# Performance work log

Hardware: AMD Instinct MI355X
Metric: run time of the kernel (lower is better)

The kernel has to match this reference:

```python
import jax, jax.numpy as jnp
import numpy as np

NEG_INF = -1e9
LRELU_SLOPE = 0.2  # torch GAT default leaky_relu negative slope


def setup_inputs() -> dict:
    key = jax.random.key(0)
    k1, k2, k3, k4, k5 = jax.random.split(key, 5)
    N, F_IN, H, DH = 4096, 1433, 8, 8  # n_nodes, in_features, n_heads, per-head dim (n_hidden=64)
    vert = jax.random.normal(k1, (N, F_IN), dtype=jnp.float32)
    edge = jax.random.randint(k2, (N, N), 0, 2, dtype=jnp.int32)  # dense adjacency mask
    W = jax.random.normal(k3, (F_IN, H * DH), dtype=jnp.float32) * 0.05
    a_l = jax.random.normal(k4, (H, DH), dtype=jnp.float32) * 0.05
    a_r = jax.random.normal(k5, (H, DH), dtype=jnp.float32) * 0.05
    return {"vert": vert, "edge": edge, "W": W, "a_l": a_l, "a_r": a_r}


def reference(vert, edge, W, a_l, a_r):
    # GAT-style edge-affinity layer (is_concat=True) + ELU; dropout is identity (eval mode).
    N = vert.shape[0]
    H, DH = a_l.shape
    g = (vert @ W).reshape(N, H, DH)                      # [N,H,Dh] projected node features
    sl = jnp.einsum('nhd,hd->nh', g, a_l)                 # source-node attention term
    sr = jnp.einsum('nhd,hd->nh', g, a_r)                 # target-node attention term
    e = sl[:, None, :] + sr[None, :, :]                   # [N,N,H]: attn([g_i || g_j])
    e = jnp.where(e >= 0, e, LRELU_SLOPE * e)             # leaky_relu
    mask = (edge != 0)[:, :, None]                        # [N,N,1]
    e = jnp.where(mask, e, NEG_INF)                       # mask non-edges
    a = jax.nn.softmax(e, axis=1)                         # normalize over neighbors j
    out = jnp.einsum('ijh,jhd->ihd', a, g).reshape(N, H * DH)  # aggregate + concat heads
    return jax.nn.elu(out)
```

## Files before the change

kernel.cpp:

```cpp
#include <hip/hip_runtime.h>
#include <hip/hip_bf16.h>

#define NN 4096
#define FIN 1433
#define NH 8
#define DH 8
#define HD 64
#define KP 1472
#define LOG2E 1.44269504f

typedef unsigned int u32;
typedef unsigned long long u64;
typedef float v4f __attribute__((ext_vector_type(4)));
typedef short bf16x4 __attribute__((ext_vector_type(4)));
typedef short bf16x8 __attribute__((ext_vector_type(8)));

static __device__ __forceinline__ short f2bf(float f) {
    union { __hip_bfloat16 h; short s; } u; u.h = __float2bfloat16(f); return u.s;
}

__global__ __launch_bounds__(256) void k_wprep(const float* __restrict__ W,
                                               short* __restrict__ Wt) {
    __shared__ float Ts[64][65];
    const int c = blockIdx.x;
    const int u = threadIdx.x;
    const int n4 = (u & 15) * 4;
    const int kr = u >> 4;
#pragma unroll
    for (int q = 0; q < 4; ++q) {
        const int kl = kr + q * 16;
        const int kg = c * 64 + kl;
        v4f v = {0.f, 0.f, 0.f, 0.f};
        if (kg < FIN) v = *(const v4f*)&W[(size_t)kg * HD + n4];
        *(v4f*)&Ts[kl][n4] = v;
    }
    __syncthreads();
    const int n = u >> 2;
    const int koff = (u & 3) * 16;
    __align__(16) short tmp[16];
#pragma unroll
    for (int r = 0; r < 16; ++r) tmp[r] = f2bf(Ts[koff + r][n]);
    *(uint4*)&Wt[(size_t)n * KP + c * 64 + koff]     = *(uint4*)&tmp[0];
    *(uint4*)&Wt[(size_t)n * KP + c * 64 + koff + 8] = *(uint4*)&tmp[8];
}

__global__ __launch_bounds__(256, 4) void k_gemm(
    const float* __restrict__ vert, const short* __restrict__ Wt,
    const float* __restrict__ al, const float* __restrict__ ar,
    short* __restrict__ gT, float* __restrict__ sl, float* __restrict__ srT)
{
    __shared__ float cacc[4][16][64];

    const int t = threadIdx.x, lane = t & 63, w = t >> 6;
    const int ml = lane & 15, q = lane >> 4;
    const int i0 = blockIdx.x * 16;
    const float* vrow = vert + (size_t)(i0 + ml) * FIN;

    v4f acc[4];
#pragma unroll
    for (int g = 0; g < 4; ++g) acc[g] = (v4f){0.f, 0.f, 0.f, 0.f};

    for (int c = w; c < 45; c += 4) {
        const int k0 = c * 32 + q * 8;
        v4f a0, a1;
        if (k0 + 7 < FIN) {
            a0 = *(const v4f*)&vrow[k0];
            a1 = *(const v4f*)&vrow[k0 + 4];
        } else {
            float tmp[8];
#pragma unroll
            for (int e = 0; e < 8; ++e)
                tmp[e] = (k0 + e < FIN) ? vrow[k0 + e] : 0.f;
            a0 = (v4f){tmp[0], tmp[1], tmp[2], tmp[3]};
            a1 = (v4f){tmp[4], tmp[5], tmp[6], tmp[7]};
        }
        const bf16x8 af = {f2bf(a0.x), f2bf(a0.y), f2bf(a0.z), f2bf(a0.w),
                           f2bf(a1.x), f2bf(a1.y), f2bf(a1.z), f2bf(a1.w)};
#pragma unroll
        for (int g = 0; g < 4; ++g) {
            const bf16x8 bf = *(const bf16x8*)&Wt[(size_t)(g * 16 + ml) * KP + k0];
            acc[g] = __builtin_amdgcn_mfma_f32_16x16x32_bf16(af, bf, acc[g], 0, 0, 0);
        }
    }

#pragma unroll
    for (int g = 0; g < 4; ++g)
#pragma unroll
        for (int r = 0; r < 4; ++r)
            cacc[w][q * 4 + r][g * 16 + ml] = acc[g][r];
    __syncthreads();

    const int m = t >> 4, n4 = (t & 15) * 4;
    v4f s = (v4f){0.f, 0.f, 0.f, 0.f};
#pragma unroll
    for (int ww = 0; ww < 4; ++ww) s += *(const v4f*)&cacc[ww][m][n4];

#pragma unroll
    for (int e = 0; e < 4; ++e)
        gT[(size_t)(n4 + e) * NN + i0 + m] = f2bf(s[e]);

    float pl = s.x * al[n4] + s.y * al[n4 + 1] + s.z * al[n4 + 2] + s.w * al[n4 + 3];
    float pr = s.x * ar[n4] + s.y * ar[n4 + 1] + s.z * ar[n4 + 2] + s.w * ar[n4 + 3];
    pl += __shfl_xor(pl, 1, 64);
    pr += __shfl_xor(pr, 1, 64);
    if ((t & 1) == 0) {
        const int h = (t & 15) >> 1;
        sl[(i0 + m) * NH + h]  = pl * LOG2E;
        srT[h * NN + i0 + m]   = pr * LOG2E;
    }
}

__global__ __launch_bounds__(256, 4) void k_attn(
    const int* __restrict__ edge, const short* __restrict__ gT,
    const float* __restrict__ sl, const float* __restrict__ srT,
    float* __restrict__ numw, float* __restrict__ denw)
{
    __shared__ __align__(16) short Gt[2][33][136];
    __shared__ __align__(16) float srs[2][4][132];
    __shared__ u32 mrow[2][16][5];

    const int t = threadIdx.x;
    const int lane = t & 63, w = t >> 6;
    const int ml = lane & 15, quad = lane >> 4;
    const int i0 = blockIdx.x * 16;
    const int hg = blockIdx.y;
    const int js = blockIdx.z;
    const int jbase = js * 2048;
    const int h  = hg * 4 + w;

    const float sli = sl[(i0 + ml) * NH + h];

    const int r2 = t >> 4, seg = (t & 15) * 8;
    const int shl = t >> 5 >= 4 ? 0 : t >> 5;
    const int sj4 = (t & 31) * 4;
    const int half = lane >> 5 ? 1 : 0;

    if (t < 16) {
        const u32 ones2 = 0x3f803f80u;
        uint4 o4 = {ones2, ones2, ones2, ones2};
        *(uint4*)&Gt[0][32][t * 8] = o4;
        *(uint4*)&Gt[1][32][t * 8] = o4;
    }

    const short* gTh = gT + (hg * 32) * NN;
    const float* srh = srT + (hg * 4) * NN;

    uint4 pg0, pg1; v4f psr; int pe[8];
    {
        pg0 = *(const uint4*)&gTh[r2 * NN + jbase + seg];
        pg1 = *(const uint4*)&gTh[(r2 + 16) * NN + jbase + seg];
        if (t < 128) psr = *(const v4f*)&srh[shl * NN + jbase + sj4];
#pragma unroll
        for (int rr = 0; rr < 4; ++rr) {
            pe[rr * 2]     = edge[(i0 + w * 4 + rr) * NN + jbase + (lane & 63)];
            pe[rr * 2 + 1] = edge[(i0 + w * 4 + rr) * NN + jbase + 64 + (lane & 63)];
        }
    }
    *(uint4*)&Gt[0][r2][seg]      = pg0;
    *(uint4*)&Gt[0][r2 + 16][seg] = pg1;
    if (t < 128) *(v4f*)&srs[0][shl][sj4] = psr;
#pragma unroll
    for (int rr = 0; rr < 4; ++rr) {
        u64 b0 = __ballot(pe[rr * 2] != 0);
        u64 b1 = __ballot(pe[rr * 2 + 1] != 0);
        if (lane == 0)  { mrow[0][w * 4 + rr][0] = (u32)b0;         mrow[0][w * 4 + rr][2] = (u32)b1; }
        if (lane == 32) { mrow[0][w * 4 + rr][1] = (u32)(b0 >> 32); mrow[0][w * 4 + rr][3] = (u32)(b1 >> 32); }
    }
    __syncthreads();

    v4f acc = {0.f, 0.f, 0.f, 0.f};

    for (int c = 0; c < 16; ++c) {
        const int cb = c & 1, nb = cb ^ 1;
        const bool pf = (c + 1) < 16;
        if (pf) {
            const int j0 = jbase + (c + 1) * 128;
            pg0 = *(const uint4*)&gTh[r2 * NN + j0 + seg];
            pg1 = *(const uint4*)&gTh[(r2 + 16) * NN + j0 + seg];
            if (t < 128) psr = *(const v4f*)&srh[shl * NN + j0 + sj4];
#pragma unroll
            for (int rr = 0; rr < 4; ++rr) {
                pe[rr * 2]     = edge[(i0 + w * 4 + rr) * NN + j0 + (lane & 63)];
                pe[rr * 2 + 1] = edge[(i0 + w * 4 + rr) * NN + j0 + 64 + (lane & 63)];
            }
        }
        const int brow = (ml < 8) ? (w * 8 + ml) : 32;
#pragma unroll
        for (int s = 0; s < 4; ++s) {
            const v4f s0 = *(const v4f*)&srs[cb][w][s * 32 + quad * 8];
            const v4f s1 = *(const v4f*)&srs[cb][w][s * 32 + quad * 8 + 4];
            const u32 mw = mrow[cb][ml][s] >> (quad * 8);
            const bf16x8 bfrag = *(const bf16x8*)&Gt[cb][brow][s * 32 + quad * 8];

            float e0 = sli + s0.x, e1 = sli + s0.y, e2 = sli + s0.z, e3 = sli + s0.w;
            float e4 = sli + s1.x, e5 = sli + s1.y, e6 = sli + s1.z, e7 = sli + s1.w;
            float p[8];
            p[0] = exp2f((mw & 1u)   ? fmaxf(e0, 0.2f * e0) : -1e9f);
            p[1] = exp2f((mw & 2u)   ? fmaxf(e1, 0.2f * e1) : -1e9f);
            p[2] = exp2f((mw & 4u)   ? fmaxf(e2, 0.2f * e2) : -1e9f);
            p[3] = exp2f((mw & 8u)   ? fmaxf(e3, 0.2f * e3) : -1e9f);
            p[4] = exp2f((mw & 16u)  ? fmaxf(e4, 0.2f * e4) : -1e9f);
            p[5] = exp2f((mw & 32u)  ? fmaxf(e5, 0.2f * e5) : -1e9f);
            p[6] = exp2f((mw & 64u)  ? fmaxf(e6, 0.2f * e6) : -1e9f);
            p[7] = exp2f((mw & 128u) ? fmaxf(e7, 0.2f * e7) : -1e9f);
            u32 w01 = __builtin_amdgcn_perm(__float_as_uint(p[1]), __float_as_uint(p[0]), 0x07060302u);
            u32 w23 = __builtin_amdgcn_perm(__float_as_uint(p[3]), __float_as_uint(p[2]), 0x07060302u);
            u32 w45 = __builtin_amdgcn_perm(__float_as_uint(p[5]), __float_as_uint(p[4]), 0x07060302u);
            u32 w67 = __builtin_amdgcn_perm(__float_as_uint(p[7]), __float_as_uint(p[6]), 0x07060302u);
            uint4 au = {w01, w23, w45, w67};
            const bf16x8 afrag = *(const bf16x8*)&au;
            acc = __builtin_amdgcn_mfma_f32_16x16x32_bf16(afrag, bfrag, acc, 0, 0, 0);
        }
        if (pf) {
            *(uint4*)&Gt[nb][r2][seg]      = pg0;
            *(uint4*)&Gt[nb][r2 + 16][seg] = pg1;
            if (t < 128) *(v4f*)&srs[nb][shl][sj4] = psr;
#pragma unroll
            for (int rr = 0; rr < 4; ++rr) {
                u64 b0 = __ballot(pe[rr * 2] != 0);
                u64 b1 = __ballot(pe[rr * 2 + 1] != 0);
                if (lane == 0)  { mrow[nb][w * 4 + rr][0] = (u32)b0;         mrow[nb][w * 4 + rr][2] = (u32)b1; }
                if (lane == 32) { mrow[nb][w * 4 + rr][1] = (u32)(b0 >> 32); mrow[nb][w * 4 + rr][3] = (u32)(b1 >> 32); }
            }
        }
        __syncthreads();
    }

    float* nw = numw + (size_t)js * NN * HD;
    float* dw = denw + (size_t)js * NN * NH;
    const int iA = i0 + quad * 4;
#pragma unroll
    for (int r = 0; r < 4; ++r) {
        if (ml < 8)       nw[(iA + r) * HD + h * 8 + ml] = acc[r];
        else if (ml == 8) dw[(iA + r) * NH + h]          = acc[r];
    }
}

__global__ __launch_bounds__(256) void k_comb(
    const float* __restrict__ numw, const float* __restrict__ denw,
    float* __restrict__ out)
{
    const int gid = blockIdx.x * 256 + threadIdx.x;
    const int i = gid >> 6, h = (gid & 63) >> 3;
    const float num = numw[gid] + numw[NN * HD + gid];
    const float den = denw[i * NH + h] + denw[NN * NH + i * NH + h];
    float x = num / den;
    out[gid] = (x > 0.f) ? x : (__expf(x) - 1.f);
}

extern "C" void kernel_launch(void* const* d_in, const int* in_sizes, int n_in,
                              void* d_out, int out_size, void* d_ws, size_t ws_size,
                              hipStream_t stream) {
    const float* vert = (const float*)d_in[0];
    const int*   edge = (const int*)d_in[1];
    const float* W    = (const float*)d_in[2];
    const float* al   = (const float*)d_in[3];
    const float* ar   = (const float*)d_in[4];
    float* out = (float*)d_out;

    char* ws = (char*)d_ws;
    short* gT   = (short*)ws;
    float* sl   = (float*)(ws + 512 * 1024);
    float* srT  = (float*)(ws + 640 * 1024);
    short* Wt   = (short*)(ws + 768 * 1024);
    float* numw = (float*)(ws + 1024 * 1024);
    float* denw = (float*)(ws + 3 * 1024 * 1024);

    hipLaunchKernelGGL(k_wprep, dim3(23), dim3(256), 0, stream, W, Wt);
    hipLaunchKernelGGL(k_gemm, dim3(NN / 16), dim3(256), 0, stream,
                       vert, Wt, al, ar, gT, sl, srT);
    hipLaunchKernelGGL(k_attn, dim3(NN / 16, 2, 2), dim3(256), 0, stream,
                       edge, gT, sl, srT, numw, denw);
    hipLaunchKernelGGL(k_comb, dim3(NN * HD / 256), dim3(256), 0, stream,
                       numw, denw, out);
}
```

Measured before the change: 172.5 us.

## Factor exp of leaky-relu scores into per-node products and split j four ways

The attention kernel now uses exp2(max(x,0.2x)) = max(exp2(x), exp2(0.2x)) and the additivity of the score. The GEMM kernel precomputes per-node exponentials (A,C for sources, B,D for targets), so the inner loop does two multiplies and a max instead of adds, leaky-relu and an exp2 per element. The neighbor dimension is also split into 4 partitions instead of 2, which gives more blocks, and the combine kernel sums four partials. The trade-offs are an extra shared-memory array and more global loads of target factors. Without max-subtraction the products may overflow or underflow if scores are large, and the reduction now touches twice as many partials.

```diff
diff --git a/kernel.cpp b/kernel.cpp
--- a/kernel.cpp
+++ b/kernel.cpp
@@ -8,6 +8,7 @@
 #define HD 64
 #define KP 1472
 #define LOG2E 1.44269504f
+#define NJS 4
 
 typedef unsigned int u32;
 typedef unsigned long long u64;
@@ -47,7 +48,8 @@
 __global__ __launch_bounds__(256, 4) void k_gemm(
     const float* __restrict__ vert, const short* __restrict__ Wt,
     const float* __restrict__ al, const float* __restrict__ ar,
-    short* __restrict__ gT, float* __restrict__ sl, float* __restrict__ srT)
+    short* __restrict__ gT, float2* __restrict__ eAC,
+    float* __restrict__ eB, float* __restrict__ eD)
 {
     __shared__ float cacc[4][16][64];
 
@@ -105,18 +107,22 @@
     pr += __shfl_xor(pr, 1, 64);
     if ((t & 1) == 0) {
         const int h = (t & 15) >> 1;
-        sl[(i0 + m) * NH + h]  = pl * LOG2E;
-        srT[h * NN + i0 + m]   = pr * LOG2E;
+        const int node = i0 + m;
+        eAC[node * NH + h] = make_float2(exp2f(pl * LOG2E), exp2f(0.2f * pl * LOG2E));
+        eB[h * NN + node] = exp2f(pr * LOG2E);
+        eD[h * NN + node] = exp2f(0.2f * pr * LOG2E);
     }
 }
 
 __global__ __launch_bounds__(256, 4) void k_attn(
     const int* __restrict__ edge, const short* __restrict__ gT,
-    const float* __restrict__ sl, const float* __restrict__ srT,
+    const float2* __restrict__ eAC, const float* __restrict__ eB,
+    const float* __restrict__ eD,
     float* __restrict__ numw, float* __restrict__ denw)
 {
     __shared__ __align__(16) short Gt[2][33][136];
-    __shared__ __align__(16) float srs[2][4][132];
+    __shared__ __align__(16) float srB[2][4][132];
+    __shared__ __align__(16) float srD[2][4][132];
     __shared__ u32 mrow[2][16][5];
 
     const int t = threadIdx.x;
@@ -125,15 +131,15 @@
     const int i0 = blockIdx.x * 16;
     const int hg = blockIdx.y;
     const int js = blockIdx.z;
-    const int jbase = js * 2048;
+    const int jbase = js * (NN / NJS);
     const int h  = hg * 4 + w;
 
-    const float sli = sl[(i0 + ml) * NH + h];
+    const float2 acv = eAC[(i0 + ml) * NH + h];
+    const float Ai = acv.x, Ci = acv.y;
 
     const int r2 = t >> 4, seg = (t & 15) * 8;
-    const int shl = t >> 5 >= 4 ? 0 : t >> 5;
+    const int shl = (t >> 5) & 3;
     const int sj4 = (t & 31) * 4;
-    const int half = lane >> 5 ? 1 : 0;
 
     if (t < 16) {
         const u32 ones2 = 0x3f803f80u;
@@ -143,22 +149,29 @@
     }
 
     const short* gTh = gT + (hg * 32) * NN;
-    const float* srh = srT + (hg * 4) * NN;
-
-    uint4 pg0, pg1; v4f psr; int pe[8];
+    const float* eBh = eB + (hg * 4) * NN;
+    const float* eDh = eD + (hg * 4) * NN;
+
+    uint4 pg0, pg1; v4f psb, psd; int pe[8];
     {
         pg0 = *(const uint4*)&gTh[r2 * NN + jbase + seg];
         pg1 = *(const uint4*)&gTh[(r2 + 16) * NN + jbase + seg];
-        if (t < 128) psr = *(const v4f*)&srh[shl * NN + jbase + sj4];
+        if (t < 128) {
+            psb = *(const v4f*)&eBh[shl * NN + jbase + sj4];
+            psd = *(const v4f*)&eDh[shl * NN + jbase + sj4];
+        }
 #pragma unroll
         for (int rr = 0; rr < 4; ++rr) {
-            pe[rr * 2]     = edge[(i0 + w * 4 + rr) * NN + jbase + (lane & 63)];
-            pe[rr * 2 + 1] = edge[(i0 + w * 4 + rr) * NN + jbase + 64 + (lane & 63)];
+            pe[rr * 2]     = edge[(i0 + w * 4 + rr) * NN + jbase + lane];
+            pe[rr * 2 + 1] = edge[(i0 + w * 4 + rr) * NN + jbase + 64 + lane];
         }
     }
     *(uint4*)&Gt[0][r2][seg]      = pg0;
     *(uint4*)&Gt[0][r2 + 16][seg] = pg1;
-    if (t < 128) *(v4f*)&srs[0][shl][sj4] = psr;
+    if (t < 128) {
+        *(v4f*)&srB[0][shl][sj4] = psb;
+        *(v4f*)&srD[0][shl][sj4] = psd;
+    }
 #pragma unroll
     for (int rr = 0; rr < 4; ++rr) {
         u64 b0 = __ballot(pe[rr * 2] != 0);
@@ -169,40 +182,44 @@
     __syncthreads();
 
     v4f acc = {0.f, 0.f, 0.f, 0.f};
-
-    for (int c = 0; c < 16; ++c) {
+    const int NCHK = (NN / NJS) / 128;
+
+    for (int c = 0; c < NCHK; ++c) {
         const int cb = c & 1, nb = cb ^ 1;
-        const bool pf = (c + 1) < 16;
+        const bool pf = (c + 1) < NCHK;
         if (pf) {
             const int j0 = jbase + (c + 1) * 128;
             pg0 = *(const uint4*)&gTh[r2 * NN + j0 + seg];
             pg1 = *(const uint4*)&gTh[(r2 + 16) * NN + j0 + seg];
-            if (t < 128) psr = *(const v4f*)&srh[shl * NN + j0 + sj4];
+            if (t < 128) {
+                psb = *(const v4f*)&eBh[shl * NN + j0 + sj4];
+                psd = *(const v4f*)&eDh[shl * NN + j0 + sj4];
+            }
 #pragma unroll
             for (int rr = 0; rr < 4; ++rr) {
-                pe[rr * 2]     = edge[(i0 + w * 4 + rr) * NN + j0 + (lane & 63)];
-                pe[rr * 2 + 1] = edge[(i0 + w * 4 + rr) * NN + j0 + 64 + (lane & 63)];
+                pe[rr * 2]     = edge[(i0 + w * 4 + rr) * NN + j0 + lane];
+                pe[rr * 2 + 1] = edge[(i0 + w * 4 + rr) * NN + j0 + 64 + lane];
             }
         }
         const int brow = (ml < 8) ? (w * 8 + ml) : 32;
 #pragma unroll
         for (int s = 0; s < 4; ++s) {
-            const v4f s0 = *(const v4f*)&srs[cb][w][s * 32 + quad * 8];
-            const v4f s1 = *(const v4f*)&srs[cb][w][s * 32 + quad * 8 + 4];
+            const v4f b0 = *(const v4f*)&srB[cb][w][s * 32 + quad * 8];
+            const v4f b1 = *(const v4f*)&srB[cb][w][s * 32 + quad * 8 + 4];
+            const v4f d0 = *(const v4f*)&srD[cb][w][s * 32 + quad * 8];
+            const v4f d1 = *(const v4f*)&srD[cb][w][s * 32 + quad * 8 + 4];
             const u32 mw = mrow[cb][ml][s] >> (quad * 8);
             const bf16x8 bfrag = *(const bf16x8*)&Gt[cb][brow][s * 32 + quad * 8];
 
-            float e0 = sli + s0.x, e1 = sli + s0.y, e2 = sli + s0.z, e3 = sli + s0.w;
-            float e4 = sli + s1.x, e5 = sli + s1.y, e6 = sli + s1.z, e7 = sli + s1.w;
             float p[8];
-            p[0] = exp2f((mw & 1u)   ? fmaxf(e0, 0.2f * e0) : -1e9f);
-            p[1] = exp2f((mw & 2u)   ? fmaxf(e1, 0.2f * e1) : -1e9f);
-            p[2] = exp2f((mw & 4u)   ? fmaxf(e2, 0.2f * e2) : -1e9f);
-            p[3] = exp2f((mw & 8u)   ? fmaxf(e3, 0.2f * e3) : -1e9f);
-            p[4] = exp2f((mw & 16u)  ? fmaxf(e4, 0.2f * e4) : -1e9f);
-            p[5] = exp2f((mw & 32u)  ? fmaxf(e5, 0.2f * e5) : -1e9f);
-            p[6] = exp2f((mw & 64u)  ? fmaxf(e6, 0.2f * e6) : -1e9f);
-            p[7] = exp2f((mw & 128u) ? fmaxf(e7, 0.2f * e7) : -1e9f);
+            p[0] = (mw & 1u)   ? fmaxf(Ai * b0.x, Ci * d0.x) : 0.f;
+            p[1] = (mw & 2u)   ? fmaxf(Ai * b0.y, Ci * d0.y) : 0.f;
+            p[2] = (mw & 4u)   ? fmaxf(Ai * b0.z, Ci * d0.z) : 0.f;
+            p[3] = (mw & 8u)   ? fmaxf(Ai * b0.w, Ci * d0.w) : 0.f;
+            p[4] = (mw & 16u)  ? fmaxf(Ai * b1.x, Ci * d1.x) : 0.f;
+            p[5] = (mw & 32u)  ? fmaxf(Ai * b1.y, Ci * d1.y) : 0.f;
+            p[6] = (mw & 64u)  ? fmaxf(Ai * b1.z, Ci * d1.z) : 0.f;
+            p[7] = (mw & 128u) ? fmaxf(Ai * b1.w, Ci * d1.w) : 0.f;
             u32 w01 = __builtin_amdgcn_perm(__float_as_uint(p[1]), __float_as_uint(p[0]), 0x07060302u);
             u32 w23 = __builtin_amdgcn_perm(__float_as_uint(p[3]), __float_as_uint(p[2]), 0x07060302u);
             u32 w45 = __builtin_amdgcn_perm(__float_as_uint(p[5]), __float_as_uint(p[4]), 0x07060302u);
@@ -214,7 +231,10 @@
         if (pf) {
             *(uint4*)&Gt[nb][r2][seg]      = pg0;
             *(uint4*)&Gt[nb][r2 + 16][seg] = pg1;
-            if (t < 128) *(v4f*)&srs[nb][shl][sj4] = psr;
+            if (t < 128) {
+                *(v4f*)&srB[nb][shl][sj4] = psb;
+                *(v4f*)&srD[nb][shl][sj4] = psd;
+            }
 #pragma unroll
             for (int rr = 0; rr < 4; ++rr) {
                 u64 b0 = __ballot(pe[rr * 2] != 0);
@@ -242,8 +262,12 @@
 {
     const int gid = blockIdx.x * 256 + threadIdx.x;
     const int i = gid >> 6, h = (gid & 63) >> 3;
-    const float num = numw[gid] + numw[NN * HD + gid];
-    const float den = denw[i * NH + h] + denw[NN * NH + i * NH + h];
+    float num = 0.f, den = 0.f;
+#pragma unroll
+    for (int s = 0; s < NJS; ++s) {
+        num += numw[s * NN * HD + gid];
+        den += denw[s * NN * NH + i * NH + h];
+    }
     float x = num / den;
     out[gid] = (x > 0.f) ? x : (__expf(x) - 1.f);
 }
@@ -259,18 +283,19 @@
     float* out = (float*)d_out;
 
     char* ws = (char*)d_ws;
-    short* gT   = (short*)ws;
-    float* sl   = (float*)(ws + 512 * 1024);
-    float* srT  = (float*)(ws + 640 * 1024);
-    short* Wt   = (short*)(ws + 768 * 1024);
-    float* numw = (float*)(ws + 1024 * 1024);
-    float* denw = (float*)(ws + 3 * 1024 * 1024);
+    short*  gT   = (short*)ws;
+    float2* eAC  = (float2*)(ws + 512 * 1024);
+    float*  eB   = (float*)(ws + 768 * 1024);
+    float*  eD   = (float*)(ws + 896 * 1024);
+    short*  Wt   = (short*)(ws + 1024 * 1024);
+    float*  numw = (float*)(ws + 1280 * 1024);
+    float*  denw = (float*)(ws + 5376 * 1024);
 
     hipLaunchKernelGGL(k_wprep, dim3(23), dim3(256), 0, stream, W, Wt);
     hipLaunchKernelGGL(k_gemm, dim3(NN / 16), dim3(256), 0, stream,
-                       vert, Wt, al, ar, gT, sl, srT);
-    hipLaunchKernelGGL(k_attn, dim3(NN / 16, 2, 2), dim3(256), 0, stream,
-                       edge, gT, sl, srT, numw, denw);
+                       vert, Wt, al, ar, gT, eAC, eB, eD);
+    hipLaunchKernelGGL(k_attn, dim3(NN / 16, 2, NJS), dim3(256), 0, stream,
+                       edge, gT, eAC, eB, eD, numw, denw);
     hipLaunchKernelGGL(k_comb, dim3(NN * HD / 256), dim3(256), 0, stream,
                        numw, denw, out);
 }
```

Measured after the change: 150.1 us. 1.15x faster.
